# Performance work log

Measured on AMD Instinct MI355X. Metric: run time of the kernel, lower is better.

Reference implementation:

```python
import jax, jax.numpy as jnp
import numpy as np

N_NODES = 100000


def gcn_conv(x, W, b, src, dst, ew, n):
    # PyG GCNConv with add_self_loops=True, symmetric normalization.
    # deg[i] = sum of incoming edge weights at i + 1.0 (self-loop weight 1)
    deg = jax.ops.segment_sum(ew, dst, num_segments=n) + 1.0
    dinv = jax.lax.rsqrt(deg)
    norm = dinv[src] * ew * dinv[dst]          # [E]
    h = x @ W                                  # [N, out]  (lin has no bias)
    msg = h[src] * norm[:, None]               # [E, out] gather + scale
    out = jax.ops.segment_sum(msg, dst, num_segments=n)
    out = out + h * (dinv * dinv)[:, None]     # self-loop contribution
    return out + b


def setup_inputs() -> dict:
    key = jax.random.key(0)
    ks = jax.random.split(key, 12)
    n, f = N_NODES, 128
    e = 1600000

    def lin_init(k, fin, fout):
        s = 1.0 / np.sqrt(fin)
        return jax.random.uniform(k, (fin, fout), jnp.float32, -s, s)

    return {
        "x": jax.random.normal(ks[0], (n, f), jnp.float32),
        "edge_index": jax.random.randint(ks[1], (2, e), 0, n, jnp.int64),
        "edge_attr": jax.random.uniform(ks[2], (e,), jnp.float32),
        "W1": lin_init(ks[3], f, 64),   "b1": jnp.zeros((64,), jnp.float32),
        "W2": lin_init(ks[4], 64, 128), "b2": jnp.zeros((128,), jnp.float32),
        "W3": lin_init(ks[5], 128, 256),"b3": jnp.zeros((256,), jnp.float32),
        "Wl1": lin_init(ks[6], 256, 128),
        "bl1": jax.random.uniform(ks[7], (128,), jnp.float32, -1/16.0, 1/16.0),
        "Wl2": lin_init(ks[8], 128, 10),
        "bl2": jax.random.uniform(ks[9], (10,), jnp.float32, -1/np.sqrt(128), 1/np.sqrt(128)),
    }


def reference(x, edge_index, edge_attr, W1, b1, W2, b2, W3, b3, Wl1, bl1, Wl2, bl2):
    src, dst = edge_index[0], edge_index[1]
    n = x.shape[0]
    h = jax.nn.relu(gcn_conv(x, W1, b1, src, dst, edge_attr, n))
    h = jax.nn.relu(gcn_conv(h, W2, b2, src, dst, edge_attr, n))
    h = jax.nn.relu(gcn_conv(h, W3, b3, src, dst, edge_attr, n))
    g = jnp.max(h, axis=0, keepdims=True)      # global_max_pool, batch=None -> [1, 256]
    g = jax.nn.relu(g @ Wl1 + bl1)
    # dropout p=0.5 is identity in eval mode
    logits = g @ Wl2 + bl2
    return jax.nn.log_softmax(logits, axis=1)
```

## Files before the change

kernel.cpp:

```cpp
#include <hip/hip_runtime.h>
#include <math.h>


typedef unsigned short u16;
typedef unsigned int   u32;
typedef unsigned long long u64;

typedef short bf16x8 __attribute__((ext_vector_type(8)));
typedef float f32x4  __attribute__((ext_vector_type(4)));

#define MAXR 64

__device__ __forceinline__ float bf2f(u16 u) {
    return __uint_as_float(((u32)u) << 16);
}
__device__ __forceinline__ u16 f2bf(float f) {
    u32 u = __float_as_uint(f);
    u32 r = (u + 0x7fffu + ((u >> 16) & 1u)) >> 16;
    return (u16)r;
}
__device__ __forceinline__ u32 pack2(float lo, float hi) {
    return (u32)f2bf(lo) | ((u32)f2bf(hi) << 16);
}


__global__ void deg_rank_kernel(const int* __restrict__ ei, const float* __restrict__ ew,
                                u64* __restrict__ pk, u16* __restrict__ rank, int E) {
    int e = blockIdx.x * blockDim.x + threadIdx.x;
    if (e < E) {
        int d = ei[E + e];
        u64 add = (1ULL << 48) | (u64)((double)ew[e] * 4294967296.0);
        u64 old = atomicAdd(&pk[(size_t)d * 8], add);
        u64 r = old >> 48;
        rank[e] = (u16)(r > 65535 ? 65535 : r);
    }
}

__global__ void scatter_kernel(const int* __restrict__ ei, const float* __restrict__ ew,
                               const u16* __restrict__ rank, uint2* __restrict__ edge2,
                               int n, int E) {
    int e = blockIdx.x * blockDim.x + threadIdx.x;
    if (e < E) {
        int r = (int)rank[e];
        if (r < MAXR) {
            int s = ei[e], d = ei[E + e];
            edge2[(size_t)r * n + d] = make_uint2((u32)s, __float_as_uint(ew[e]));
        }
    }
}

__global__ void finish_deg_kernel(const u64* __restrict__ pk, float* __restrict__ dinv, int n) {
    int i = blockIdx.x * blockDim.x + threadIdx.x;
    if (i < n) {
        double deg = (double)(pk[(size_t)i * 8] & ((1ULL << 48) - 1)) * (1.0 / 4294967296.0);
        dinv[i] = rsqrtf((float)deg + 1.0f);
    }
}

template<int FIN, int FOUT>
__global__ void wconv_kernel(const float* __restrict__ W, u16* __restrict__ Wf) {
    int t = blockIdx.x;
    int s = blockIdx.y;
    int l = threadIdx.x;
    int col = t * 16 + (l & 15);
    int k0 = s * 32 + 8 * (l >> 4);
    u32 packed[4];
    for (int jj = 0; jj < 4; ++jj) {
        u16 lo = f2bf(W[(size_t)(k0 + 2 * jj) * FOUT + col]);
        u16 hi = f2bf(W[(size_t)(k0 + 2 * jj + 1) * FOUT + col]);
        packed[jj] = (u32)lo | ((u32)hi << 16);
    }
    u32* dst = (u32*)&Wf[(((size_t)t * (FIN / 32) + s) * 64 + l) * 8];
    dst[0] = packed[0]; dst[1] = packed[1]; dst[2] = packed[2]; dst[3] = packed[3];
}

template<int FIN, int FOUT>
__global__ __launch_bounds__(256)
void gemm0_kernel(const float* __restrict__ x, const float* __restrict__ dinv,
                  const u16* __restrict__ Wf, u16* __restrict__ Y, int n) {
    constexpr int KS = FIN / 32;
    constexpr int NT = FOUT / 16;
    constexpr int Q8 = FIN / 8;
    __shared__ u16 Asw[4][KS][64][8];
    int tid = threadIdx.x;
    int gbase = blockIdx.x * 64;

    for (int idx = tid; idx < 64 * Q8; idx += 256) {
        int m = idx / Q8, q = idx - m * Q8;
        int gn = gbase + m;
        uint4 o = make_uint4(0, 0, 0, 0);
        if (gn < n) {
            float di = dinv[gn];
            const float4* p = reinterpret_cast<const float4*>(&x[(size_t)gn * FIN + q * 8]);
            float4 a = p[0], b = p[1];
            o.x = pack2(di * a.x, di * a.y);
            o.y = pack2(di * a.z, di * a.w);
            o.z = pack2(di * b.x, di * b.y);
            o.w = pack2(di * b.z, di * b.w);
        }
        *reinterpret_cast<uint4*>(&Asw[m >> 4][q >> 2][((q & 3) << 4) | (m & 15)][0]) = o;
    }
    __syncthreads();

    int w = tid >> 6, lane = tid & 63;
    int nodeq = gbase + w * 16 + ((lane >> 4) << 2);

    bf16x8 a[KS];
    #pragma unroll
    for (int s = 0; s < KS; ++s)
        a[s] = *reinterpret_cast<const bf16x8*>(&Asw[w][s][lane][0]);

    int col0 = lane & 15;
    #pragma unroll
    for (int t = 0; t < NT; ++t) {
        f32x4 acc = {0.f, 0.f, 0.f, 0.f};
        #pragma unroll
        for (int s = 0; s < KS; ++s) {
            bf16x8 bf = *reinterpret_cast<const bf16x8*>(&Wf[(((size_t)t * KS + s) * 64 + lane) * 8]);
            acc = __builtin_amdgcn_mfma_f32_16x16x32_bf16(a[s], bf, acc, 0, 0, 0);
        }
        int col = t * 16 + col0;
        #pragma unroll
        for (int r = 0; r < 4; ++r) {
            int node = nodeq + r;
            if (node < n) Y[(size_t)node * FOUT + col] = f2bf(acc[r]);
        }
    }
}

template<int F>
__global__ __launch_bounds__(256)
void agg_epi_kernel(const u16* __restrict__ Y, const u64* __restrict__ pk,
                    const uint2* __restrict__ edge2, const float* __restrict__ dinv,
                    const float* __restrict__ b, u16* __restrict__ Rout, int n) {
    constexpr int TPN = F / 8;
    constexpr int NPB = 256 / TPN;
    int t = threadIdx.x;
    int node = blockIdx.x * NPB + t / TPN;
    if (node >= n) return;
    int j8 = (t % TPN) * 8;
    int cnt = (int)(pk[(size_t)node * 8] >> 48);
    if (cnt > MAXR) cnt = MAXR;
    float di = dinv[node];

    uint4 sv = *reinterpret_cast<const uint4*>(&Y[(size_t)node * F + j8]);
    float acc0, acc1, acc2, acc3, acc4, acc5, acc6, acc7;
    acc0 = bf2f((u16)sv.x);  acc1 = bf2f((u16)(sv.x >> 16));
    acc2 = bf2f((u16)sv.y);  acc3 = bf2f((u16)(sv.y >> 16));
    acc4 = bf2f((u16)sv.z);  acc5 = bf2f((u16)(sv.z >> 16));
    acc6 = bf2f((u16)sv.w);  acc7 = bf2f((u16)(sv.w >> 16));

    const uint2* ecol = edge2 + node;
    int e = 0;
    for (; e + 4 <= cnt; e += 4) {
        uint2 ed0 = ecol[(size_t)e * n];
        uint2 ed1 = ecol[(size_t)(e + 1) * n];
        uint2 ed2 = ecol[(size_t)(e + 2) * n];
        uint2 ed3 = ecol[(size_t)(e + 3) * n];
        uint4 h0 = *reinterpret_cast<const uint4*>(&Y[(size_t)ed0.x * F + j8]);
        uint4 h1 = *reinterpret_cast<const uint4*>(&Y[(size_t)ed1.x * F + j8]);
        uint4 h2 = *reinterpret_cast<const uint4*>(&Y[(size_t)ed2.x * F + j8]);
        uint4 h3 = *reinterpret_cast<const uint4*>(&Y[(size_t)ed3.x * F + j8]);
        float w0 = __uint_as_float(ed0.y);
        float w1 = __uint_as_float(ed1.y);
        float w2 = __uint_as_float(ed2.y);
        float w3 = __uint_as_float(ed3.y);
        acc0 += w0 * bf2f((u16)h0.x) + w1 * bf2f((u16)h1.x) + w2 * bf2f((u16)h2.x) + w3 * bf2f((u16)h3.x);
        acc1 += w0 * bf2f((u16)(h0.x >> 16)) + w1 * bf2f((u16)(h1.x >> 16)) + w2 * bf2f((u16)(h2.x >> 16)) + w3 * bf2f((u16)(h3.x >> 16));
        acc2 += w0 * bf2f((u16)h0.y) + w1 * bf2f((u16)h1.y) + w2 * bf2f((u16)h2.y) + w3 * bf2f((u16)h3.y);
        acc3 += w0 * bf2f((u16)(h0.y >> 16)) + w1 * bf2f((u16)(h1.y >> 16)) + w2 * bf2f((u16)(h2.y >> 16)) + w3 * bf2f((u16)(h3.y >> 16));
        acc4 += w0 * bf2f((u16)h0.z) + w1 * bf2f((u16)h1.z) + w2 * bf2f((u16)h2.z) + w3 * bf2f((u16)h3.z);
        acc5 += w0 * bf2f((u16)(h0.z >> 16)) + w1 * bf2f((u16)(h1.z >> 16)) + w2 * bf2f((u16)(h2.z >> 16)) + w3 * bf2f((u16)(h3.z >> 16));
        acc6 += w0 * bf2f((u16)h0.w) + w1 * bf2f((u16)h1.w) + w2 * bf2f((u16)h2.w) + w3 * bf2f((u16)h3.w);
        acc7 += w0 * bf2f((u16)(h0.w >> 16)) + w1 * bf2f((u16)(h1.w >> 16)) + w2 * bf2f((u16)(h2.w >> 16)) + w3 * bf2f((u16)(h3.w >> 16));
    }
    for (; e < cnt; ++e) {
        uint2 ed = ecol[(size_t)e * n];
        float w = __uint_as_float(ed.y);
        uint4 hv = *reinterpret_cast<const uint4*>(&Y[(size_t)ed.x * F + j8]);
        acc0 += w * bf2f((u16)hv.x);  acc1 += w * bf2f((u16)(hv.x >> 16));
        acc2 += w * bf2f((u16)hv.y);  acc3 += w * bf2f((u16)(hv.y >> 16));
        acc4 += w * bf2f((u16)hv.z);  acc5 += w * bf2f((u16)(hv.z >> 16));
        acc6 += w * bf2f((u16)hv.w);  acc7 += w * bf2f((u16)(hv.w >> 16));
    }

    const float4* bp = reinterpret_cast<const float4*>(&b[j8]);
    float4 b0 = bp[0], b1v = bp[1];
    uint4 o;
    o.x = pack2(di * fmaxf(di * acc0 + b0.x, 0.f), di * fmaxf(di * acc1 + b0.y, 0.f));
    o.y = pack2(di * fmaxf(di * acc2 + b0.z, 0.f), di * fmaxf(di * acc3 + b0.w, 0.f));
    o.z = pack2(di * fmaxf(di * acc4 + b1v.x, 0.f), di * fmaxf(di * acc5 + b1v.y, 0.f));
    o.w = pack2(di * fmaxf(di * acc6 + b1v.z, 0.f), di * fmaxf(di * acc7 + b1v.w, 0.f));
    *reinterpret_cast<uint4*>(&Rout[(size_t)node * F + j8]) = o;
}

template<int FIN, int FOUT, bool FUSE_MAX, bool SCALE_OUT>
__global__ __launch_bounds__(256)
void fused_layer_kernel(const u16* __restrict__ R, const u64* __restrict__ pk,
                        const uint2* __restrict__ edge2, const float* __restrict__ dinv,
                        const u16* __restrict__ Wf, const float* __restrict__ b,
                        u16* __restrict__ Rout, float* __restrict__ g, int n) {
    constexpr int KS  = FIN / 32;
    constexpr int NT  = FOUT / 16;
    constexpr int TPN = FIN / 8;
    constexpr int NPB = 256 / TPN;
    constexpr int NIT = 64 / NPB;
    __shared__ u16 Asw[4][KS][64][8];
    __shared__ int gsm[256];
    int tid = threadIdx.x;
    int gbase = blockIdx.x * 64;

    if (FUSE_MAX) gsm[tid] = 0;

    int sub = tid / TPN;
    int q   = tid % TPN;
    #pragma unroll
    for (int it = 0; it < NIT; ++it) {
        int m = it * NPB + sub;
        int node = gbase + m;
        float acc[8];
        #pragma unroll
        for (int j = 0; j < 8; ++j) acc[j] = 0.f;

        if (node < n) {
            int cnt = (int)(pk[(size_t)node * 8] >> 48);
            if (cnt > MAXR) cnt = MAXR;
            float di = dinv[node];

            auto fmadd = [&](float w, uint4 h) {
                acc[0] += w * bf2f((u16)h.x);  acc[1] += w * bf2f((u16)(h.x >> 16));
                acc[2] += w * bf2f((u16)h.y);  acc[3] += w * bf2f((u16)(h.y >> 16));
                acc[4] += w * bf2f((u16)h.z);  acc[5] += w * bf2f((u16)(h.z >> 16));
                acc[6] += w * bf2f((u16)h.w);  acc[7] += w * bf2f((u16)(h.w >> 16));
            };

            uint4 sv = *reinterpret_cast<const uint4*>(&R[(size_t)node * FIN + q * 8]);
            fmadd(1.0f, sv);

            const uint2* ecol = edge2 + node;
            int e = 0;
            for (; e + 4 <= cnt; e += 4) {
                uint2 ed0 = ecol[(size_t)e * n];
                uint2 ed1 = ecol[(size_t)(e + 1) * n];
                uint2 ed2 = ecol[(size_t)(e + 2) * n];
                uint2 ed3 = ecol[(size_t)(e + 3) * n];
                uint4 h0 = *reinterpret_cast<const uint4*>(&R[(size_t)ed0.x * FIN + q * 8]);
                uint4 h1 = *reinterpret_cast<const uint4*>(&R[(size_t)ed1.x * FIN + q * 8]);
                uint4 h2 = *reinterpret_cast<const uint4*>(&R[(size_t)ed2.x * FIN + q * 8]);
                uint4 h3 = *reinterpret_cast<const uint4*>(&R[(size_t)ed3.x * FIN + q * 8]);
                fmadd(__uint_as_float(ed0.y), h0);
                fmadd(__uint_as_float(ed1.y), h1);
                fmadd(__uint_as_float(ed2.y), h2);
                fmadd(__uint_as_float(ed3.y), h3);
            }
            for (; e < cnt; ++e) {
                uint2 ed = ecol[(size_t)e * n];
                uint4 hv = *reinterpret_cast<const uint4*>(&R[(size_t)ed.x * FIN + q * 8]);
                fmadd(__uint_as_float(ed.y), hv);
            }

            #pragma unroll
            for (int j = 0; j < 8; ++j) acc[j] *= di;
        }

        uint4 o;
        o.x = pack2(acc[0], acc[1]);
        o.y = pack2(acc[2], acc[3]);
        o.z = pack2(acc[4], acc[5]);
        o.w = pack2(acc[6], acc[7]);
        *reinterpret_cast<uint4*>(&Asw[m >> 4][q >> 2][((q & 3) << 4) | (m & 15)][0]) = o;
    }
    __syncthreads();

    int w = tid >> 6, lane = tid & 63;
    int nodeq = gbase + w * 16 + ((lane >> 4) << 2);

    bf16x8 a[KS];
    #pragma unroll
    for (int s = 0; s < KS; ++s)
        a[s] = *reinterpret_cast<const bf16x8*>(&Asw[w][s][lane][0]);

    float dv[4];
    if (SCALE_OUT) {
        #pragma unroll
        for (int r = 0; r < 4; ++r) {
            int node = nodeq + r;
            dv[r] = (node < n) ? dinv[node] : 0.f;
        }
    }

    int col0 = lane & 15;
    #pragma unroll
    for (int t = 0; t < NT; ++t) {
        f32x4 acc = {0.f, 0.f, 0.f, 0.f};
        #pragma unroll
        for (int s = 0; s < KS; ++s) {
            bf16x8 bf = *reinterpret_cast<const bf16x8*>(&Wf[(((size_t)t * KS + s) * 64 + lane) * 8]);
            acc = __builtin_amdgcn_mfma_f32_16x16x32_bf16(a[s], bf, acc, 0, 0, 0);
        }
        int col = t * 16 + col0;
        float bb = b[col];
        if (FUSE_MAX) {
            float ml = 0.0f;
            #pragma unroll
            for (int r = 0; r < 4; ++r) {
                int node = nodeq + r;
                float v = acc[r] + bb;
                if (node < n) ml = fmaxf(ml, v);
            }
            ml = fmaxf(ml, __shfl_xor(ml, 16));
            ml = fmaxf(ml, __shfl_xor(ml, 32));
            if ((lane >> 4) == 0) atomicMax(&gsm[col], __float_as_int(ml));
        } else {
            #pragma unroll
            for (int r = 0; r < 4; ++r) {
                int node = nodeq + r;
                if (node < n) {
                    float v = fmaxf(acc[r] + bb, 0.0f);
                    if (SCALE_OUT) v *= dv[r];
                    Rout[(size_t)node * FOUT + col] = f2bf(v);
                }
            }
        }
    }
    if (FUSE_MAX) {
        __syncthreads();
        atomicMax(&((int*)g)[tid], gsm[tid]);
    }
}


__global__ void head_kernel(const float* __restrict__ g, const float* __restrict__ Wl1,
                            const float* __restrict__ bl1, const float* __restrict__ Wl2,
                            const float* __restrict__ bl2, float* __restrict__ out) {
    __shared__ float gs[256];
    __shared__ float ys[128];
    __shared__ float ls[10];
    int t = threadIdx.x;
    gs[t] = g[t];
    __syncthreads();
    if (t < 128) {
        float acc = bl1[t];
        for (int k = 0; k < 256; ++k) acc += gs[k] * Wl1[k * 128 + t];
        ys[t] = fmaxf(acc, 0.0f);
    }
    __syncthreads();
    if (t < 10) {
        float acc = bl2[t];
        for (int j = 0; j < 128; ++j) acc += ys[j] * Wl2[j * 10 + t];
        ls[t] = acc;
    }
    __syncthreads();
    if (t == 0) {
        float m = ls[0];
        for (int c = 1; c < 10; ++c) m = fmaxf(m, ls[c]);
        float se = 0.0f;
        for (int c = 0; c < 10; ++c) se += expf(ls[c] - m);
        float lse = logf(se);
        for (int c = 0; c < 10; ++c) out[c] = ls[c] - m - lse;
    }
}


static inline int cdiv(int a, int b) { return (a + b - 1) / b; }

extern "C" void kernel_launch(void* const* d_in, const int* in_sizes, int n_in,
                              void* d_out, int out_size, void* d_ws, size_t ws_size,
                              hipStream_t stream) {
    const float* x   = (const float*)d_in[0];
    const int*   ei  = (const int*)d_in[1];
    const float* ew  = (const float*)d_in[2];
    const float* W1  = (const float*)d_in[3];
    const float* b1  = (const float*)d_in[4];
    const float* W2  = (const float*)d_in[5];
    const float* b2  = (const float*)d_in[6];
    const float* W3  = (const float*)d_in[7];
    const float* b3  = (const float*)d_in[8];
    const float* Wl1 = (const float*)d_in[9];
    const float* bl1 = (const float*)d_in[10];
    const float* Wl2 = (const float*)d_in[11];
    const float* bl2 = (const float*)d_in[12];

    const int n = in_sizes[0] / 128;
    const int E = in_sizes[1] / 2;

    char* p = (char*)d_ws;
    auto alloc = [&](size_t bytes) { char* q = p; p += (bytes + 255) & ~(size_t)255; return q; };
    u64*   pk    = (u64*)  alloc((size_t)n * 64);
    float* dinv  = (float*)alloc((size_t)n * 4);
    u16*   rank  = (u16*)  alloc((size_t)E * 2);
    uint2* edge2 = (uint2*)alloc((size_t)MAXR * n * 8);
    u16*   y1    = (u16*)  alloc((size_t)n * 64 * 2);
    u16*   r2    = (u16*)  alloc((size_t)n * 64 * 2);
    u16*   r3    = (u16*)  alloc((size_t)n * 128 * 2);
    u16*   W1f   = (u16*)  alloc((size_t)128 * 64 * 2);
    u16*   W2f   = (u16*)  alloc((size_t)64 * 128 * 2);
    u16*   W3f   = (u16*)  alloc((size_t)128 * 256 * 2);
    float* g     = (float*)alloc(256 * 4);

    hipMemsetAsync(pk, 0, (size_t)n * 64, stream);
    hipMemsetAsync(g,  0, 256 * 4, stream);

    int eb = cdiv(E, 256);
    deg_rank_kernel<<<eb, 256, 0, stream>>>(ei, ew, pk, rank, E);
    scatter_kernel<<<eb, 256, 0, stream>>>(ei, ew, rank, edge2, n, E);
    finish_deg_kernel<<<cdiv(n, 256), 256, 0, stream>>>(pk, dinv, n);

    wconv_kernel<128, 64><<<dim3(64 / 16, 128 / 32), 64, 0, stream>>>(W1, W1f);
    wconv_kernel<64, 128><<<dim3(128 / 16, 64 / 32), 64, 0, stream>>>(W2, W2f);
    wconv_kernel<128, 256><<<dim3(256 / 16, 128 / 32), 64, 0, stream>>>(W3, W3f);

    gemm0_kernel<128, 64><<<cdiv(n, 64), 256, 0, stream>>>(x, dinv, W1f, y1, n);
    agg_epi_kernel<64><<<cdiv(n, 32), 256, 0, stream>>>(y1, pk, edge2, dinv, b1, r2, n);
    fused_layer_kernel<64, 128, false, true><<<cdiv(n, 64), 256, 0, stream>>>(r2, pk, edge2, dinv, W2f, b2, r3, nullptr, n);
    fused_layer_kernel<128, 256, true, false><<<cdiv(n, 64), 256, 0, stream>>>(r3, pk, edge2, dinv, W3f, b3, nullptr, g, n);

    head_kernel<<<1, 256, 0, stream>>>(g, Wl1, bl1, Wl2, bl2, (float*)d_out);
}
```

Baseline: 311.3 us.

## Merge preprocessing into one mega kernel, transpose edge layout, fold dinv into edge weights

Merges degree/rank counting, weight conversion and the first GEMM (with inline W1 conversion, no dinv prescale) into one heterogeneous launch. Edge slots switch from rank-major to node-major layout and store ew*dinv[src], so the source-side normalization moves from activations into the edge weights. The fused layers now process 32 nodes per block, with waves splitting the output columns. This reduces launches and makes per-node edge reads contiguous, at the cost of fewer nodes per block and W1 reloaded from global memory in every GEMM block.

```diff
diff --git a/kernel.cpp b/kernel.cpp
--- a/kernel.cpp
+++ b/kernel.cpp
@@ -24,106 +24,115 @@
 }
 
 
-__global__ void deg_rank_kernel(const int* __restrict__ ei, const float* __restrict__ ew,
-                                u64* __restrict__ pk, u16* __restrict__ rank, int E) {
-    int e = blockIdx.x * blockDim.x + threadIdx.x;
-    if (e < E) {
-        int d = ei[E + e];
-        u64 add = (1ULL << 48) | (u64)((double)ew[e] * 4294967296.0);
-        u64 old = atomicAdd(&pk[(size_t)d * 8], add);
-        u64 r = old >> 48;
-        rank[e] = (u16)(r > 65535 ? 65535 : r);
+__global__ __launch_bounds__(256, 8)
+void mega_kernel(const int* __restrict__ ei, const float* __restrict__ ew,
+                 u64* __restrict__ pk, u16* __restrict__ rank, int E,
+                 const float* __restrict__ x, const float* __restrict__ W1,
+                 u16* __restrict__ y1,
+                 const float* __restrict__ W2, u16* __restrict__ W2f,
+                 const float* __restrict__ W3, u16* __restrict__ W3f,
+                 int n, int gb, int wb) {
+    __shared__ u16 Asw[4][4][64][8];
+    int bid = blockIdx.x;
+    int tid = threadIdx.x;
+
+    if (bid < gb) {
+        int gbase = bid * 64;
+        for (int idx = tid; idx < 64 * 16; idx += 256) {
+            int m = idx >> 4, q = idx & 15;
+            int gn = gbase + m;
+            uint4 o = make_uint4(0, 0, 0, 0);
+            if (gn < n) {
+                const float4* p = reinterpret_cast<const float4*>(&x[(size_t)gn * 128 + q * 8]);
+                float4 a = p[0], b = p[1];
+                o.x = pack2(a.x, a.y); o.y = pack2(a.z, a.w);
+                o.z = pack2(b.x, b.y); o.w = pack2(b.z, b.w);
+            }
+            *reinterpret_cast<uint4*>(&Asw[m >> 4][q >> 2][((q & 3) << 4) | (m & 15)][0]) = o;
+        }
+        __syncthreads();
+        int w = tid >> 6, lane = tid & 63;
+        int nodeq = gbase + w * 16 + ((lane >> 4) << 2);
+        bf16x8 a[4];
+        #pragma unroll
+        for (int s = 0; s < 4; ++s)
+            a[s] = *reinterpret_cast<const bf16x8*>(&Asw[w][s][lane][0]);
+        int col0 = lane & 15;
+        int krow = 8 * (lane >> 4);
+        #pragma unroll
+        for (int t = 0; t < 4; ++t) {
+            int col = t * 16 + col0;
+            f32x4 acc = {0.f, 0.f, 0.f, 0.f};
+            #pragma unroll
+            for (int s = 0; s < 4; ++s) {
+                int k0 = s * 32 + krow;
+                bf16x8 bf;
+                u32* bw = reinterpret_cast<u32*>(&bf);
+                #pragma unroll
+                for (int jj = 0; jj < 4; ++jj)
+                    bw[jj] = pack2(W1[(size_t)(k0 + 2 * jj) * 64 + col],
+                                   W1[(size_t)(k0 + 2 * jj + 1) * 64 + col]);
+                acc = __builtin_amdgcn_mfma_f32_16x16x32_bf16(a[s], bf, acc, 0, 0, 0);
+            }
+            #pragma unroll
+            for (int r = 0; r < 4; ++r) {
+                int node = nodeq + r;
+                if (node < n) y1[(size_t)node * 64 + col] = f2bf(acc[r]);
+            }
+        }
+    } else if (bid < gb + wb) {
+        int u = (bid - gb) * 4 + (tid >> 6);
+        int l = tid & 63;
+        if (u < 16) {
+            int t = u >> 1, s = u & 1;
+            int col = t * 16 + (l & 15);
+            int k0 = s * 32 + 8 * (l >> 4);
+            u32* dst = (u32*)&W2f[(((size_t)t * 2 + s) * 64 + l) * 8];
+            #pragma unroll
+            for (int jj = 0; jj < 4; ++jj)
+                dst[jj] = pack2(W2[(size_t)(k0 + 2 * jj) * 128 + col],
+                                W2[(size_t)(k0 + 2 * jj + 1) * 128 + col]);
+        } else {
+            int v = u - 16;
+            int t = v >> 2, s = v & 3;
+            int col = t * 16 + (l & 15);
+            int k0 = s * 32 + 8 * (l >> 4);
+            u32* dst = (u32*)&W3f[(((size_t)t * 4 + s) * 64 + l) * 8];
+            #pragma unroll
+            for (int jj = 0; jj < 4; ++jj)
+                dst[jj] = pack2(W3[(size_t)(k0 + 2 * jj) * 256 + col],
+                                W3[(size_t)(k0 + 2 * jj + 1) * 256 + col]);
+        }
+    } else {
+        int e = (bid - gb - wb) * 256 + tid;
+        if (e < E) {
+            int d = ei[E + e];
+            u64 add = (1ULL << 48) | (u64)((double)ew[e] * 4294967296.0);
+            u64 old = atomicAdd(&pk[(size_t)d * 8], add);
+            u64 r = old >> 48;
+            rank[e] = (u16)(r > 65535 ? 65535 : r);
+        }
+    }
+}
+
+__global__ void finish_deg_kernel(const u64* __restrict__ pk, float* __restrict__ dinv, int n) {
+    int i = blockIdx.x * blockDim.x + threadIdx.x;
+    if (i < n) {
+        double deg = (double)(pk[(size_t)i * 8] & ((1ULL << 48) - 1)) * (1.0 / 4294967296.0);
+        dinv[i] = rsqrtf((float)deg + 1.0f);
     }
 }
 
 __global__ void scatter_kernel(const int* __restrict__ ei, const float* __restrict__ ew,
-                               const u16* __restrict__ rank, uint2* __restrict__ edge2,
-                               int n, int E) {
+                               const u16* __restrict__ rank, const float* __restrict__ dinv,
+                               uint2* __restrict__ edge2, int n, int E) {
     int e = blockIdx.x * blockDim.x + threadIdx.x;
     if (e < E) {
         int r = (int)rank[e];
         if (r < MAXR) {
             int s = ei[e], d = ei[E + e];
-            edge2[(size_t)r * n + d] = make_uint2((u32)s, __float_as_uint(ew[e]));
-        }
-    }
-}
-
-__global__ void finish_deg_kernel(const u64* __restrict__ pk, float* __restrict__ dinv, int n) {
-    int i = blockIdx.x * blockDim.x + threadIdx.x;
-    if (i < n) {
-        double deg = (double)(pk[(size_t)i * 8] & ((1ULL << 48) - 1)) * (1.0 / 4294967296.0);
-        dinv[i] = rsqrtf((float)deg + 1.0f);
-    }
-}
-
-template<int FIN, int FOUT>
-__global__ void wconv_kernel(const float* __restrict__ W, u16* __restrict__ Wf) {
-    int t = blockIdx.x;
-    int s = blockIdx.y;
-    int l = threadIdx.x;
-    int col = t * 16 + (l & 15);
-    int k0 = s * 32 + 8 * (l >> 4);
-    u32 packed[4];
-    for (int jj = 0; jj < 4; ++jj) {
-        u16 lo = f2bf(W[(size_t)(k0 + 2 * jj) * FOUT + col]);
-        u16 hi = f2bf(W[(size_t)(k0 + 2 * jj + 1) * FOUT + col]);
-        packed[jj] = (u32)lo | ((u32)hi << 16);
-    }
-    u32* dst = (u32*)&Wf[(((size_t)t * (FIN / 32) + s) * 64 + l) * 8];
-    dst[0] = packed[0]; dst[1] = packed[1]; dst[2] = packed[2]; dst[3] = packed[3];
-}
-
-template<int FIN, int FOUT>
-__global__ __launch_bounds__(256)
-void gemm0_kernel(const float* __restrict__ x, const float* __restrict__ dinv,
-                  const u16* __restrict__ Wf, u16* __restrict__ Y, int n) {
-    constexpr int KS = FIN / 32;
-    constexpr int NT = FOUT / 16;
-    constexpr int Q8 = FIN / 8;
-    __shared__ u16 Asw[4][KS][64][8];
-    int tid = threadIdx.x;
-    int gbase = blockIdx.x * 64;
-
-    for (int idx = tid; idx < 64 * Q8; idx += 256) {
-        int m = idx / Q8, q = idx - m * Q8;
-        int gn = gbase + m;
-        uint4 o = make_uint4(0, 0, 0, 0);
-        if (gn < n) {
-            float di = dinv[gn];
-            const float4* p = reinterpret_cast<const float4*>(&x[(size_t)gn * FIN + q * 8]);
-            float4 a = p[0], b = p[1];
-            o.x = pack2(di * a.x, di * a.y);
-            o.y = pack2(di * a.z, di * a.w);
-            o.z = pack2(di * b.x, di * b.y);
-            o.w = pack2(di * b.z, di * b.w);
-        }
-        *reinterpret_cast<uint4*>(&Asw[m >> 4][q >> 2][((q & 3) << 4) | (m & 15)][0]) = o;
-    }
-    __syncthreads();
-
-    int w = tid >> 6, lane = tid & 63;
-    int nodeq = gbase + w * 16 + ((lane >> 4) << 2);
-
-    bf16x8 a[KS];
-    #pragma unroll
-    for (int s = 0; s < KS; ++s)
-        a[s] = *reinterpret_cast<const bf16x8*>(&Asw[w][s][lane][0]);
-
-    int col0 = lane & 15;
-    #pragma unroll
-    for (int t = 0; t < NT; ++t) {
-        f32x4 acc = {0.f, 0.f, 0.f, 0.f};
-        #pragma unroll
-        for (int s = 0; s < KS; ++s) {
-            bf16x8 bf = *reinterpret_cast<const bf16x8*>(&Wf[(((size_t)t * KS + s) * 64 + lane) * 8]);
-            acc = __builtin_amdgcn_mfma_f32_16x16x32_bf16(a[s], bf, acc, 0, 0, 0);
-        }
-        int col = t * 16 + col0;
-        #pragma unroll
-        for (int r = 0; r < 4; ++r) {
-            int node = nodeq + r;
-            if (node < n) Y[(size_t)node * FOUT + col] = f2bf(acc[r]);
+            float wp = ew[e] * dinv[s];
+            edge2[(size_t)d * MAXR + r] = make_uint2((u32)s, __float_as_uint(wp));
         }
     }
 }
@@ -145,18 +154,18 @@
 
     uint4 sv = *reinterpret_cast<const uint4*>(&Y[(size_t)node * F + j8]);
     float acc0, acc1, acc2, acc3, acc4, acc5, acc6, acc7;
-    acc0 = bf2f((u16)sv.x);  acc1 = bf2f((u16)(sv.x >> 16));
-    acc2 = bf2f((u16)sv.y);  acc3 = bf2f((u16)(sv.y >> 16));
-    acc4 = bf2f((u16)sv.z);  acc5 = bf2f((u16)(sv.z >> 16));
-    acc6 = bf2f((u16)sv.w);  acc7 = bf2f((u16)(sv.w >> 16));
-
-    const uint2* ecol = edge2 + node;
+    acc0 = di * bf2f((u16)sv.x);  acc1 = di * bf2f((u16)(sv.x >> 16));
+    acc2 = di * bf2f((u16)sv.y);  acc3 = di * bf2f((u16)(sv.y >> 16));
+    acc4 = di * bf2f((u16)sv.z);  acc5 = di * bf2f((u16)(sv.z >> 16));
+    acc6 = di * bf2f((u16)sv.w);  acc7 = di * bf2f((u16)(sv.w >> 16));
+
+    const uint2* ecol = edge2 + (size_t)node * MAXR;
     int e = 0;
     for (; e + 4 <= cnt; e += 4) {
-        uint2 ed0 = ecol[(size_t)e * n];
-        uint2 ed1 = ecol[(size_t)(e + 1) * n];
-        uint2 ed2 = ecol[(size_t)(e + 2) * n];
-        uint2 ed3 = ecol[(size_t)(e + 3) * n];
+        uint2 ed0 = ecol[e];
+        uint2 ed1 = ecol[e + 1];
+        uint2 ed2 = ecol[e + 2];
+        uint2 ed3 = ecol[e + 3];
         uint4 h0 = *reinterpret_cast<const uint4*>(&Y[(size_t)ed0.x * F + j8]);
         uint4 h1 = *reinterpret_cast<const uint4*>(&Y[(size_t)ed1.x * F + j8]);
         uint4 h2 = *reinterpret_cast<const uint4*>(&Y[(size_t)ed2.x * F + j8]);
@@ -175,7 +184,7 @@
         acc7 += w0 * bf2f((u16)(h0.w >> 16)) + w1 * bf2f((u16)(h1.w >> 16)) + w2 * bf2f((u16)(h2.w >> 16)) + w3 * bf2f((u16)(h3.w >> 16));
     }
     for (; e < cnt; ++e) {
-        uint2 ed = ecol[(size_t)e * n];
+        uint2 ed = ecol[e];
         float w = __uint_as_float(ed.y);
         uint4 hv = *reinterpret_cast<const uint4*>(&Y[(size_t)ed.x * F + j8]);
         acc0 += w * bf2f((u16)hv.x);  acc1 += w * bf2f((u16)(hv.x >> 16));
@@ -187,28 +196,28 @@
     const float4* bp = reinterpret_cast<const float4*>(&b[j8]);
     float4 b0 = bp[0], b1v = bp[1];
     uint4 o;
-    o.x = pack2(di * fmaxf(di * acc0 + b0.x, 0.f), di * fmaxf(di * acc1 + b0.y, 0.f));
-    o.y = pack2(di * fmaxf(di * acc2 + b0.z, 0.f), di * fmaxf(di * acc3 + b0.w, 0.f));
-    o.z = pack2(di * fmaxf(di * acc4 + b1v.x, 0.f), di * fmaxf(di * acc5 + b1v.y, 0.f));
-    o.w = pack2(di * fmaxf(di * acc6 + b1v.z, 0.f), di * fmaxf(di * acc7 + b1v.w, 0.f));
+    o.x = pack2(fmaxf(di * acc0 + b0.x, 0.f),  fmaxf(di * acc1 + b0.y, 0.f));
+    o.y = pack2(fmaxf(di * acc2 + b0.z, 0.f),  fmaxf(di * acc3 + b0.w, 0.f));
+    o.z = pack2(fmaxf(di * acc4 + b1v.x, 0.f), fmaxf(di * acc5 + b1v.y, 0.f));
+    o.w = pack2(fmaxf(di * acc6 + b1v.z, 0.f), fmaxf(di * acc7 + b1v.w, 0.f));
     *reinterpret_cast<uint4*>(&Rout[(size_t)node * F + j8]) = o;
 }
 
-template<int FIN, int FOUT, bool FUSE_MAX, bool SCALE_OUT>
+template<int FIN, int FOUT, bool FUSE_MAX>
 __global__ __launch_bounds__(256)
-void fused_layer_kernel(const u16* __restrict__ R, const u64* __restrict__ pk,
-                        const uint2* __restrict__ edge2, const float* __restrict__ dinv,
-                        const u16* __restrict__ Wf, const float* __restrict__ b,
-                        u16* __restrict__ Rout, float* __restrict__ g, int n) {
+void fused32_kernel(const u16* __restrict__ R, const u64* __restrict__ pk,
+                    const uint2* __restrict__ edge2, const float* __restrict__ dinv,
+                    const u16* __restrict__ Wf, const float* __restrict__ b,
+                    u16* __restrict__ Rout, float* __restrict__ g, int n) {
     constexpr int KS  = FIN / 32;
     constexpr int NT  = FOUT / 16;
     constexpr int TPN = FIN / 8;
     constexpr int NPB = 256 / TPN;
-    constexpr int NIT = 64 / NPB;
-    __shared__ u16 Asw[4][KS][64][8];
+    constexpr int NIT = 32 / NPB;
+    __shared__ u16 Asw[2][KS][64][8];
     __shared__ int gsm[256];
     int tid = threadIdx.x;
-    int gbase = blockIdx.x * 64;
+    int gbase = blockIdx.x * 32;
 
     if (FUSE_MAX) gsm[tid] = 0;
 
@@ -235,15 +244,15 @@
             };
 
             uint4 sv = *reinterpret_cast<const uint4*>(&R[(size_t)node * FIN + q * 8]);
-            fmadd(1.0f, sv);
-
-            const uint2* ecol = edge2 + node;
+            fmadd(di, sv);
+
+            const uint2* ecol = edge2 + (size_t)node * MAXR;
             int e = 0;
             for (; e + 4 <= cnt; e += 4) {
-                uint2 ed0 = ecol[(size_t)e * n];
-                uint2 ed1 = ecol[(size_t)(e + 1) * n];
-                uint2 ed2 = ecol[(size_t)(e + 2) * n];
-                uint2 ed3 = ecol[(size_t)(e + 3) * n];
+                uint2 ed0 = ecol[e];
+                uint2 ed1 = ecol[e + 1];
+                uint2 ed2 = ecol[e + 2];
+                uint2 ed3 = ecol[e + 3];
                 uint4 h0 = *reinterpret_cast<const uint4*>(&R[(size_t)ed0.x * FIN + q * 8]);
                 uint4 h1 = *reinterpret_cast<const uint4*>(&R[(size_t)ed1.x * FIN + q * 8]);
                 uint4 h2 = *reinterpret_cast<const uint4*>(&R[(size_t)ed2.x * FIN + q * 8]);
@@ -254,7 +263,7 @@
                 fmadd(__uint_as_float(ed3.y), h3);
             }
             for (; e < cnt; ++e) {
-                uint2 ed = ecol[(size_t)e * n];
+                uint2 ed = ecol[e];
                 uint4 hv = *reinterpret_cast<const uint4*>(&R[(size_t)ed.x * FIN + q * 8]);
                 fmadd(__uint_as_float(ed.y), hv);
             }
@@ -273,25 +282,18 @@
     __syncthreads();
 
     int w = tid >> 6, lane = tid & 63;
-    int nodeq = gbase + w * 16 + ((lane >> 4) << 2);
+    int mt = w & 1, nh = w >> 1;
+    int nodeq = gbase + mt * 16 + ((lane >> 4) << 2);
 
     bf16x8 a[KS];
     #pragma unroll
     for (int s = 0; s < KS; ++s)
-        a[s] = *reinterpret_cast<const bf16x8*>(&Asw[w][s][lane][0]);
-
-    float dv[4];
-    if (SCALE_OUT) {
-        #pragma unroll
-        for (int r = 0; r < 4; ++r) {
-            int node = nodeq + r;
-            dv[r] = (node < n) ? dinv[node] : 0.f;
-        }
-    }
+        a[s] = *reinterpret_cast<const bf16x8*>(&Asw[mt][s][lane][0]);
 
     int col0 = lane & 15;
     #pragma unroll
-    for (int t = 0; t < NT; ++t) {
+    for (int i = 0; i < NT / 2; ++i) {
+        int t = nh * (NT / 2) + i;
         f32x4 acc = {0.f, 0.f, 0.f, 0.f};
         #pragma unroll
         for (int s = 0; s < KS; ++s) {
@@ -317,7 +319,6 @@
                 int node = nodeq + r;
                 if (node < n) {
                     float v = fmaxf(acc[r] + bb, 0.0f);
-                    if (SCALE_OUT) v *= dv[r];
                     Rout[(size_t)node * FOUT + col] = f2bf(v);
                 }
             }
@@ -389,11 +390,10 @@
     u64*   pk    = (u64*)  alloc((size_t)n * 64);
     float* dinv  = (float*)alloc((size_t)n * 4);
     u16*   rank  = (u16*)  alloc((size_t)E * 2);
-    uint2* edge2 = (uint2*)alloc((size_t)MAXR * n * 8);
+    uint2* edge2 = (uint2*)alloc((size_t)n * MAXR * 8);
     u16*   y1    = (u16*)  alloc((size_t)n * 64 * 2);
     u16*   r2    = (u16*)  alloc((size_t)n * 64 * 2);
     u16*   r3    = (u16*)  alloc((size_t)n * 128 * 2);
-    u16*   W1f   = (u16*)  alloc((size_t)128 * 64 * 2);
     u16*   W2f   = (u16*)  alloc((size_t)64 * 128 * 2);
     u16*   W3f   = (u16*)  alloc((size_t)128 * 256 * 2);
     float* g     = (float*)alloc(256 * 4);
@@ -402,18 +402,17 @@
     hipMemsetAsync(g,  0, 256 * 4, stream);
 
     int eb = cdiv(E, 256);
-    deg_rank_kernel<<<eb, 256, 0, stream>>>(ei, ew, pk, rank, E);
-    scatter_kernel<<<eb, 256, 0, stream>>>(ei, ew, rank, edge2, n, E);
+    int gb = cdiv(n, 64);
+    int wb = 20;
+    mega_kernel<<<gb + wb + eb, 256, 0, stream>>>(ei, ew, pk, rank, E,
+                                                  x, W1, y1, W2, W2f, W3, W3f,
+                                                  n, gb, wb);
     finish_deg_kernel<<<cdiv(n, 256), 256, 0, stream>>>(pk, dinv, n);
-
-    wconv_kernel<128, 64><<<dim3(64 / 16, 128 / 32), 64, 0, stream>>>(W1, W1f);
-    wconv_kernel<64, 128><<<dim3(128 / 16, 64 / 32), 64, 0, stream>>>(W2, W2f);
-    wconv_kernel<128, 256><<<dim3(256 / 16, 128 / 32), 64, 0, stream>>>(W3, W3f);
-
-    gemm0_kernel<128, 64><<<cdiv(n, 64), 256, 0, stream>>>(x, dinv, W1f, y1, n);
+    scatter_kernel<<<eb, 256, 0, stream>>>(ei, ew, rank, dinv, edge2, n, E);
+
     agg_epi_kernel<64><<<cdiv(n, 32), 256, 0, stream>>>(y1, pk, edge2, dinv, b1, r2, n);
-    fused_layer_kernel<64, 128, false, true><<<cdiv(n, 64), 256, 0, stream>>>(r2, pk, edge2, dinv, W2f, b2, r3, nullptr, n);
-    fused_layer_kernel<128, 256, true, false><<<cdiv(n, 64), 256, 0, stream>>>(r3, pk, edge2, dinv, W3f, b3, nullptr, g, n);
+    fused32_kernel<64, 128, false><<<cdiv(n, 32), 256, 0, stream>>>(r2, pk, edge2, dinv, W2f, b2, r3, nullptr, n);
+    fused32_kernel<128, 256, true><<<cdiv(n, 32), 256, 0, stream>>>(r3, pk, edge2, dinv, W3f, b3, nullptr, g, n);
 
     head_kernel<<<1, 256, 0, stream>>>(g, Wl1, bl1, Wl2, bl2, (float*)d_out);
 }
```

Result: no change. 310.6 us (-0.2%).
